# Kernel optimization log

Measured on AMD Instinct MI355X. Metric: run time of the kernel, lower is better.

The kernel has to match this reference:

```python
import jax, jax.numpy as jnp
import numpy as np

B, E, DIN, H, D, T = 16, 512, 1024, 8, 128, 3
NEG = -1e30
LRELU_SLOPE = 0.2


def setup_inputs() -> dict:
    key = jax.random.key(0)
    ks = jax.random.split(key, 6)
    x = jax.random.normal(ks[0], (B, E, DIN), dtype=jnp.float32)
    adj = jax.random.randint(ks[1], (B, E, E), 0, 4, dtype=jnp.int32)  # 0=no edge, 1..3 edge types
    node_mask = jnp.ones((B, E, 1), dtype=jnp.float32)
    W = jax.random.normal(ks[2], (H, T, DIN, D), dtype=jnp.float32) * 0.02
    a1 = jax.random.normal(ks[3], (H, T, D), dtype=jnp.float32) * 0.02  # a[:d]
    a2 = jax.random.normal(ks[4], (H, T, D), dtype=jnp.float32) * 0.02  # a[d:]
    return {"x": x, "adj": adj, "node_mask": node_mask, "W": W, "a1": a1, "a2": a2}


def reference(x, adj, node_mask, W, a1, a2):
    # h per head/type: [H, T, B, E, D]
    h = jnp.einsum('bei,htid->htbed', x, W)
    # a(cat(h_i, h_j)) = h_i . a1 + h_j . a2 (linear, no bias)
    left = jnp.einsum('htbed,htd->htbe', h, a1)   # [H,T,B,E]
    right = jnp.einsum('htbed,htd->htbe', h, a2)  # [H,T,B,E]
    score = left[..., :, None] + right[..., None, :]             # [H,T,B,E,E]
    score = jnp.where(score > 0, score, LRELU_SLOPE * score)      # LeakyReLU(0.2)
    type_ids = (jnp.arange(T, dtype=adj.dtype) + 1).reshape(1, T, 1, 1, 1)
    # sum over types: only positions where adj == type contribute
    scores = jnp.sum(jnp.where(adj[None, None] == type_ids, score, 0.0), axis=1)  # [H,B,E,E]
    scores = jnp.where(adj[None] > 0, scores, NEG)
    coefs = jax.nn.softmax(scores, axis=-1)                       # [H,B,E,E]
    # original bug (faithful): h used in aggregation is from the LAST edge type
    h_last = h[:, -1] * node_mask[None]                           # [H,B,E,D]
    out = jnp.einsum('hbef,hbfd->hbed', coefs, h_last)            # [H,B,E,D]
    out = jnp.transpose(out, (1, 2, 0, 3)).reshape(B, E, H * D)   # concat heads
    return jax.nn.relu(out)
```

## Files before the change

### kernel.cpp

```cpp
#include <hip/hip_runtime.h>

typedef __attribute__((ext_vector_type(8))) _Float16 half8;
typedef __attribute__((ext_vector_type(8))) unsigned short u16x8;
typedef __attribute__((ext_vector_type(4))) unsigned short u16x4;
typedef __attribute__((ext_vector_type(4))) float f32x4;

#define NEGV (-1e30f)


__device__ __forceinline__ unsigned short f2h(float f) {
    union { _Float16 h; unsigned short u; } c;
    c.h = (_Float16)f;
    return c.u;
}
__device__ __forceinline__ float h2f(unsigned short u) {
    union { _Float16 h; unsigned short u; } c;
    c.u = u;
    return (float)c.h;
}

__global__ __launch_bounds__(256) void prep_kernel(const int* __restrict__ adj,
                                                   const float* __restrict__ W,
                                                   const float* __restrict__ a1,
                                                   const float* __restrict__ a2,
                                                   unsigned short* __restrict__ Bf,
                                                   unsigned char* __restrict__ adjB) {
    __shared__ float tile[64 * 133];
    const int bid = blockIdx.x;
    const int tid = threadIdx.x;

    if (bid < 1024) {
        const int idx = bid * 256 + tid;
        const int4* s = (const int4*)(adj + (size_t)idx * 16);
        int4 v0 = s[0], v1 = s[1], v2 = s[2], v3 = s[3];
        union { unsigned char c[16]; int4 v; } o;
        o.c[0] = (unsigned char)v0.x; o.c[1] = (unsigned char)v0.y;
        o.c[2] = (unsigned char)v0.z; o.c[3] = (unsigned char)v0.w;
        o.c[4] = (unsigned char)v1.x; o.c[5] = (unsigned char)v1.y;
        o.c[6] = (unsigned char)v1.z; o.c[7] = (unsigned char)v1.w;
        o.c[8] = (unsigned char)v2.x; o.c[9] = (unsigned char)v2.y;
        o.c[10] = (unsigned char)v2.z; o.c[11] = (unsigned char)v2.w;
        o.c[12] = (unsigned char)v3.x; o.c[13] = (unsigned char)v3.y;
        o.c[14] = (unsigned char)v3.z; o.c[15] = (unsigned char)v3.w;
        *(int4*)(adjB + (size_t)idx * 16) = o.v;
    } else if (bid < 1152) {
        const int pb = bid - 1024;
        const int kt = pb & 15, h = pb >> 4;
        const int k0 = kt * 64;
        const float* wsrc = W + ((size_t)((h * 3 + 2) * 1024) + k0) * 128;

        #pragma unroll
        for (int rep = 0; rep < 8; ++rep) {
            int idx = rep * 256 + tid;
            int k = idx >> 5, dc = (idx & 31) * 4;
            float4 v = *(const float4*)(wsrc + (size_t)k * 128 + dc);
            tile[k * 133 + dc + 0] = v.x;
            tile[k * 133 + dc + 1] = v.y;
            tile[k * 133 + dc + 2] = v.z;
            tile[k * 133 + dc + 3] = v.w;
        }
        __syncthreads();
        #pragma unroll
        for (int rep = 0; rep < 4; ++rep) {
            int idx = rep * 256 + tid;
            int d = idx >> 3, kc = (idx & 7) * 8;
            u16x8 vh;
            #pragma unroll
            for (int q = 0; q < 8; ++q) vh[q] = f2h(tile[(kc + q) * 133 + d]);
            *(u16x8*)(Bf + (size_t)(h * 128 + d) * 1024 + k0 + kc) = vh;
        }
    } else if (bid < 1536) {
        const int pb = bid - 1152;
        const int kt = pb & 15, ht = pb >> 4;
        const int h = ht & 7, t = ht >> 3;
        const int k0 = kt * 64;
        const float* wsrc = W + ((size_t)((h * 3 + t) * 1024) + k0) * 128;

        #pragma unroll
        for (int rep = 0; rep < 8; ++rep) {
            int idx = rep * 256 + tid;
            int k = idx >> 5, dc = (idx & 31) * 4;
            float4 v = *(const float4*)(wsrc + (size_t)k * 128 + dc);
            tile[k * 133 + dc + 0] = v.x;
            tile[k * 133 + dc + 1] = v.y;
            tile[k * 133 + dc + 2] = v.z;
            tile[k * 133 + dc + 3] = v.w;
        }
        __syncthreads();
        if (tid < 128) {
            const int k = tid & 63, s = tid >> 6;
            const float* ar = (s ? a2 : a1) + (h * 3 + t) * 128;
            float acc = 0.f;
            #pragma unroll 4
            for (int d = 0; d < 128; ++d) acc += tile[k * 133 + d] * ar[d];
            Bf[(size_t)(1024 + s * 24 + t * 8 + h) * 1024 + k0 + k] = f2h(acc);
        }
    } else {
        const int n = 1072 + (bid - 1536);
        *(unsigned long long*)(Bf + (size_t)n * 1024 + tid * 4) = 0ull;
    }
}

__global__ __launch_bounds__(256, 3) void mgemm(const float* __restrict__ X,
                                                const unsigned short* __restrict__ Bf,
                                                const float* __restrict__ nm,
                                                unsigned short* __restrict__ Vt,
                                                float* __restrict__ LR) {
    __shared__ unsigned short Ah[2][128 * 32];
    __shared__ unsigned short Bfs[2][128 * 32];

    const int bid = blockIdx.x;
    const int swz = (bid & 7) * 72 + (bid >> 3);
    const int nt = swz % 9, mt = swz / 9;
    const int n0 = nt * 128, m0 = mt * 128;

    const int tid = threadIdx.x;
    const int lane = tid & 63, w = tid >> 6;
    const int wr = w >> 1, wc = w & 1;
    const int fr = lane & 15, fq = lane >> 4;

    f32x4 acc[4][4];
    #pragma unroll
    for (int m = 0; m < 4; ++m)
        #pragma unroll
        for (int n = 0; n < 4; ++n) acc[m][n] = (f32x4){0.f, 0.f, 0.f, 0.f};

    const int arow = tid >> 1, ahalf = tid & 1;
    const float* xs = X + (size_t)(m0 + arow) * 1024 + ahalf * 16;
    const int aoff = arow * 32 + ahalf * 16;

#define GLDB(kk, buf) do {                                                        \
        _Pragma("unroll")                                                          \
        for (int q_ = 0; q_ < 2; ++q_) {                                           \
            const int s_ = q_ * 256 + tid;                                         \
            const int brow_ = s_ >> 2, bkb_ = s_ & 3;                              \
            const unsigned short* g_ = Bf + (size_t)(n0 + brow_) * 1024 + (kk) + bkb_ * 8; \
            unsigned short* d_ = &Bfs[buf][(q_ * 256 + w * 64) * 8];               \
            __builtin_amdgcn_global_load_lds(                                      \
                (const __attribute__((address_space(1))) void*)g_,                 \
                (__attribute__((address_space(3))) void*)d_, 16, 0, 0);            \
        }                                                                          \
    } while (0)

#define CONVA(xa_, xb_, xc_, xd_, buf) do {                                       \
        float xf_[16] = {(xa_).x, (xa_).y, (xa_).z, (xa_).w,                       \
                         (xb_).x, (xb_).y, (xb_).z, (xb_).w,                       \
                         (xc_).x, (xc_).y, (xc_).z, (xc_).w,                       \
                         (xd_).x, (xd_).y, (xd_).z, (xd_).w};                      \
        u16x8 v0_, v1_;                                                            \
        _Pragma("unroll")                                                          \
        for (int i_ = 0; i_ < 8; ++i_) v0_[i_] = f2h(xf_[i_]);                     \
        _Pragma("unroll")                                                          \
        for (int i_ = 0; i_ < 8; ++i_) v1_[i_] = f2h(xf_[8 + i_]);                 \
        *(u16x8*)(&Ah[buf][aoff]) = v0_;                                           \
        *(u16x8*)(&Ah[buf][aoff + 8]) = v1_;                                       \
    } while (0)

    GLDB(0, 0);
    {
        float4 xa = *(const float4*)(xs);
        float4 xb = *(const float4*)(xs + 4);
        float4 xc = *(const float4*)(xs + 8);
        float4 xd = *(const float4*)(xs + 12);
        CONVA(xa, xb, xc, xd, 0);
    }
    __syncthreads();

    for (int k0 = 0; k0 < 1024; k0 += 32) {
        const int cur = (k0 >> 5) & 1;
        const int nxt = cur ^ 1;
        const bool more = (k0 < 992);

        float4 xa, xb, xc, xd;
        if (more) {
            GLDB(k0 + 32, nxt);
            xa = *(const float4*)(xs + k0 + 32);
            xb = *(const float4*)(xs + k0 + 36);
            xc = *(const float4*)(xs + k0 + 40);
            xd = *(const float4*)(xs + k0 + 44);
        }

        half8 am[4], bn[4];
        #pragma unroll
        for (int m = 0; m < 4; ++m)
            am[m] = *(half8*)(&Ah[cur][(wr * 64 + m * 16 + fr) * 32 + fq * 8]);
        #pragma unroll
        for (int n = 0; n < 4; ++n)
            bn[n] = *(half8*)(&Bfs[cur][(wc * 64 + n * 16 + fr) * 32 + fq * 8]);
        #pragma unroll
        for (int m = 0; m < 4; ++m)
            #pragma unroll
            for (int n = 0; n < 4; ++n)
                acc[m][n] = __builtin_amdgcn_mfma_f32_16x16x32_f16(am[m], bn[n], acc[m][n], 0, 0, 0);

        if (more) {
            CONVA(xa, xb, xc, xd, nxt);
        }

        __syncthreads();
    }
#undef GLDB
#undef CONVA

    if (nt < 8) {
        const int b_ = (mt * 128) >> 9;
        const int jb0 = (mt & 3) * 128;
        unsigned short* vtw = Vt + (size_t)(nt * 16 + b_) * 128 * 512;
        #pragma unroll
        for (int m = 0; m < 4; ++m) {
            const int jb = jb0 + wr * 64 + m * 16 + fq * 4;
            float mk[4];
            #pragma unroll
            for (int r = 0; r < 4; ++r)
                mk[r] = nm[m0 + wr * 64 + m * 16 + fq * 4 + r];
            #pragma unroll
            for (int n = 0; n < 4; ++n) {
                const int d = wc * 64 + n * 16 + fr;
                u16x4 pk;
                #pragma unroll
                for (int r = 0; r < 4; ++r) pk[r] = f2h(acc[m][n][r] * mk[r]);
                *(u16x4*)(vtw + (size_t)d * 512 + jb) = pk;
            }
        }
    } else {
        #pragma unroll
        for (int m = 0; m < 4; ++m) {
            #pragma unroll
            for (int r = 0; r < 4; ++r) {
                const int R = m0 + wr * 64 + m * 16 + fq * 4 + r;
                #pragma unroll
                for (int n = 0; n < 4; ++n) {
                    const int c = wc * 64 + n * 16 + fr;
                    if (c < 48) LR[(size_t)c * 8192 + R] = acc[m][n][r];
                }
            }
        }
    }
}

__global__ __launch_bounds__(256, 4) void attn_kernel(const unsigned short* __restrict__ Vt,
                                                      const float* __restrict__ LR,
                                                      const unsigned char* __restrict__ adjB,
                                                      float* __restrict__ out) {
    __shared__ __align__(16) unsigned short Vb[2][16 * 512];
    __shared__ __align__(16) float rt[3 * 512];

    const int bid = blockIdx.x;
    const int itg = bid >> 7, hb = bid & 127, h = hb >> 4, b = hb & 15;
    const int tid = threadIdx.x, w = tid >> 6, lane = tid & 63;
    const int fr = lane & 15, fq = lane >> 4;
    const int i0 = (itg * 4 + w) * 16;
    const int fq8 = fq * 8;

    for (int idx = tid; idx < 1536; idx += 256) {
        int t = idx >> 9, j = idx & 511;
        rt[idx] = LR[(size_t)(24 + t * 8 + h) * 8192 + b * 512 + j];
    }
    const float lf0 = LR[(size_t)(h) * 8192 + b * 512 + i0 + fr];
    const float lf1 = LR[(size_t)(8 + h) * 8192 + b * 512 + i0 + fr];
    const float lf2 = LR[(size_t)(16 + h) * 8192 + b * 512 + i0 + fr];
    const unsigned char* arow = adjB + (size_t)(b * 512 + i0 + fr) * 512;
    const unsigned short* vt = Vt + (size_t)(h * 16 + b) * 128 * 512;

#define STAGE_V(bufp, os_) do {                                                   \
        _Pragma("unroll")                                                          \
        for (int q_ = 0; q_ < 4; ++q_) {                                           \
            const int nh_ = q_ * 4 + w;                                            \
            const unsigned short* src_ = vt + (size_t)((nh_ >> 1) * 16 + fr) * 512 \
                                          + (os_) * 64 + (nh_ & 1) * 32 + fq8;     \
            unsigned short* dst_ = (bufp) + nh_ * 512;                             \
            __builtin_amdgcn_global_load_lds(                                      \
                (const __attribute__((address_space(1))) void*)src_,               \
                (__attribute__((address_space(3))) void*)dst_, 16, 0, 0);          \
        }                                                                          \
    } while (0)

    STAGE_V(&Vb[0][0], 0);
    uint2 aA = *(const uint2*)(arow + fq8);
    uint2 aB = *(const uint2*)(arow + fq8 + 32);

    f32x4 acc[8];
    #pragma unroll
    for (int n = 0; n < 8; ++n) acc[n] = (f32x4){0.f, 0.f, 0.f, 0.f};
    float rsum = 0.f;

    __syncthreads();

    #pragma unroll 1
    for (int os = 0; os < 8; ++os) {
        unsigned short* vb = &Vb[os & 1][0];
        if (os < 7) STAGE_V(&Vb[(os & 1) ^ 1][0], os + 1);

        const int jA = os * 64 + fq8;
        const int jB = jA + 32;

        u16x8 vhA, vhB;
        {
            float4 r0a = *(const float4*)(rt + jA), r0b = *(const float4*)(rt + jA + 4);
            float4 r1a = *(const float4*)(rt + 512 + jA), r1b = *(const float4*)(rt + 512 + jA + 4);
            float4 r2a = *(const float4*)(rt + 1024 + jA), r2b = *(const float4*)(rt + 1024 + jA + 4);
            float e0[8] = {r0a.x, r0a.y, r0a.z, r0a.w, r0b.x, r0b.y, r0b.z, r0b.w};
            float e1[8] = {r1a.x, r1a.y, r1a.z, r1a.w, r1b.x, r1b.y, r1b.z, r1b.w};
            float e2[8] = {r2a.x, r2a.y, r2a.z, r2a.w, r2b.x, r2b.y, r2b.z, r2b.w};
            #pragma unroll
            for (int q = 0; q < 8; ++q) {
                unsigned av = ((q < 4 ? aA.x : aA.y) >> (8 * (q & 3))) & 255u;
                float sb = (av == 1u) ? (lf0 + e0[q])
                         : (av == 2u) ? (lf1 + e1[q]) : (lf2 + e2[q]);
                float sv = fmaxf(sb, 0.f) + 0.2f * fminf(sb, 0.f);
                float p = (av != 0u) ? __expf(sv) : 0.f;
                rsum += p;
                vhA[q] = f2h(p);
            }
        }
        {
            float4 r0a = *(const float4*)(rt + jB), r0b = *(const float4*)(rt + jB + 4);
            float4 r1a = *(const float4*)(rt + 512 + jB), r1b = *(const float4*)(rt + 512 + jB + 4);
            float4 r2a = *(const float4*)(rt + 1024 + jB), r2b = *(const float4*)(rt + 1024 + jB + 4);
            float e0[8] = {r0a.x, r0a.y, r0a.z, r0a.w, r0b.x, r0b.y, r0b.z, r0b.w};
            float e1[8] = {r1a.x, r1a.y, r1a.z, r1a.w, r1b.x, r1b.y, r1b.z, r1b.w};
            float e2[8] = {r2a.x, r2a.y, r2a.z, r2a.w, r2b.x, r2b.y, r2b.z, r2b.w};
            #pragma unroll
            for (int q = 0; q < 8; ++q) {
                unsigned av = ((q < 4 ? aB.x : aB.y) >> (8 * (q & 3))) & 255u;
                float sb = (av == 1u) ? (lf0 + e0[q])
                         : (av == 2u) ? (lf1 + e1[q]) : (lf2 + e2[q]);
                float sv = fmaxf(sb, 0.f) + 0.2f * fminf(sb, 0.f);
                float p = (av != 0u) ? __expf(sv) : 0.f;
                rsum += p;
                vhB[q] = f2h(p);
            }
        }
        if (os < 7) {
            aA = *(const uint2*)(arow + (os + 1) * 64 + fq8);
            aB = *(const uint2*)(arow + (os + 1) * 64 + fq8 + 32);
        }

        half8 ahA = *(half8*)&vhA, ahB = *(half8*)&vhB;

        #pragma unroll
        for (int n = 0; n < 8; ++n) {
            half8 vA = *(half8*)(vb + (n * 2 + 0) * 512 + lane * 8);
            half8 vB = *(half8*)(vb + (n * 2 + 1) * 512 + lane * 8);
            acc[n] = __builtin_amdgcn_mfma_f32_16x16x32_f16(ahA, vA, acc[n], 0, 0, 0);
            acc[n] = __builtin_amdgcn_mfma_f32_16x16x32_f16(ahB, vB, acc[n], 0, 0, 0);
        }
        __syncthreads();
    }
#undef STAGE_V

    rsum += __shfl_xor(rsum, 16);
    rsum += __shfl_xor(rsum, 32);

    #pragma unroll
    for (int rr = 0; rr < 4; ++rr) {
        const int row = fq * 4 + rr;
        const float inv = 1.0f / __shfl(rsum, row);
        #pragma unroll
        for (int n = 0; n < 8; ++n) {
            out[(size_t)(b * 512 + i0 + row) * 1024 + h * 128 + n * 16 + fr] =
                fmaxf(acc[n][rr] * inv, 0.f);
        }
    }
}

extern "C" void kernel_launch(void* const* d_in, const int* in_sizes, int n_in,
                              void* d_out, int out_size, void* d_ws, size_t ws_size,
                              hipStream_t stream) {
    const float* x   = (const float*)d_in[0];
    const int*   adj = (const int*)d_in[1];
    const float* nm  = (const float*)d_in[2];
    const float* W   = (const float*)d_in[3];
    const float* a1  = (const float*)d_in[4];
    const float* a2  = (const float*)d_in[5];
    float* out = (float*)d_out;
    char* wsb = (char*)d_ws;

    unsigned short* Bf   = (unsigned short*)(wsb);
    float*          LR   = (float*)(wsb + 21495808);
    unsigned short* Vt   = (unsigned short*)(wsb + 23068672);
    unsigned char*  adjB = (unsigned char*)(wsb + 39845888);

    hipLaunchKernelGGL(prep_kernel, dim3(1616), dim3(256), 0, stream, adj, W, a1, a2, Bf, adjB);
    hipLaunchKernelGGL(mgemm, dim3(576), dim3(256), 0, stream, x, Bf, nm, Vt, LR);
    hipLaunchKernelGGL(attn_kernel, dim3(1024), dim3(256), 0, stream, Vt, LR, adjB, out);
}
```

Before: 108.6 us.

## Unroll GEMM K-loop by two with register-prefetched x and partial vmcnt barriers

Restructures the projection GEMM main loop into a manually unrolled two-stage pipeline with static buffer indices. The x fp32 loads are now issued one stage further ahead, into a second register set. __syncthreads is replaced by inline s_waitcnt vmcnt(4) plus s_barrier, so the x loads still in flight need not drain at every barrier. sched_barrier fences pin instruction order. This aims to hide global-load latency behind the MFMAs, at the cost of more VGPRs and a fragile hand-counted vmcnt that must match the number of outstanding loads.

```diff
diff --git a/kernel.cpp b/kernel.cpp
--- a/kernel.cpp
+++ b/kernel.cpp
@@ -156,51 +156,76 @@
         *(u16x8*)(&Ah[buf][aoff + 8]) = v1_;                                       \
     } while (0)
 
+#define COMPUTE(buf) do {                                                         \
+        half8 am_[4], bn_[4];                                                      \
+        _Pragma("unroll")                                                          \
+        for (int m_ = 0; m_ < 4; ++m_)                                             \
+            am_[m_] = *(half8*)(&Ah[buf][(wr * 64 + m_ * 16 + fr) * 32 + fq * 8]); \
+        _Pragma("unroll")                                                          \
+        for (int n_ = 0; n_ < 4; ++n_)                                             \
+            bn_[n_] = *(half8*)(&Bfs[buf][(wc * 64 + n_ * 16 + fr) * 32 + fq * 8]);\
+        _Pragma("unroll")                                                          \
+        for (int m_ = 0; m_ < 4; ++m_)                                             \
+            _Pragma("unroll")                                                      \
+            for (int n_ = 0; n_ < 4; ++n_)                                         \
+                acc[m_][n_] = __builtin_amdgcn_mfma_f32_16x16x32_f16(am_[m_], bn_[n_], acc[m_][n_], 0, 0, 0); \
+    } while (0)
+
+#define PIPE_BAR4() asm volatile("s_waitcnt vmcnt(4) lgkmcnt(0)\n\ts_barrier" ::: "memory")
+#define PIPE_BAR0() asm volatile("s_waitcnt vmcnt(0) lgkmcnt(0)\n\ts_barrier" ::: "memory")
+
+    float4 x0a, x0b, x0c, x0d, x1a, x1b, x1c, x1d;
+
+    x0a = *(const float4*)(xs);
+    x0b = *(const float4*)(xs + 4);
+    x0c = *(const float4*)(xs + 8);
+    x0d = *(const float4*)(xs + 12);
+    __builtin_amdgcn_sched_barrier(0);
     GLDB(0, 0);
-    {
-        float4 xa = *(const float4*)(xs);
-        float4 xb = *(const float4*)(xs + 4);
-        float4 xc = *(const float4*)(xs + 8);
-        float4 xd = *(const float4*)(xs + 12);
-        CONVA(xa, xb, xc, xd, 0);
-    }
-    __syncthreads();
-
-    for (int k0 = 0; k0 < 1024; k0 += 32) {
-        const int cur = (k0 >> 5) & 1;
-        const int nxt = cur ^ 1;
-        const bool more = (k0 < 992);
-
-        float4 xa, xb, xc, xd;
-        if (more) {
-            GLDB(k0 + 32, nxt);
-            xa = *(const float4*)(xs + k0 + 32);
-            xb = *(const float4*)(xs + k0 + 36);
-            xc = *(const float4*)(xs + k0 + 40);
-            xd = *(const float4*)(xs + k0 + 44);
-        }
-
-        half8 am[4], bn[4];
-        #pragma unroll
-        for (int m = 0; m < 4; ++m)
-            am[m] = *(half8*)(&Ah[cur][(wr * 64 + m * 16 + fr) * 32 + fq * 8]);
-        #pragma unroll
-        for (int n = 0; n < 4; ++n)
-            bn[n] = *(half8*)(&Bfs[cur][(wc * 64 + n * 16 + fr) * 32 + fq * 8]);
-        #pragma unroll
-        for (int m = 0; m < 4; ++m)
-            #pragma unroll
-            for (int n = 0; n < 4; ++n)
-                acc[m][n] = __builtin_amdgcn_mfma_f32_16x16x32_f16(am[m], bn[n], acc[m][n], 0, 0, 0);
-
-        if (more) {
-            CONVA(xa, xb, xc, xd, nxt);
-        }
-
-        __syncthreads();
-    }
+    __builtin_amdgcn_sched_barrier(0);
+    CONVA(x0a, x0b, x0c, x0d, 0);
+    x1a = *(const float4*)(xs + 32);
+    x1b = *(const float4*)(xs + 36);
+    x1c = *(const float4*)(xs + 40);
+    x1d = *(const float4*)(xs + 44);
+    PIPE_BAR4();
+
+    for (int kk = 0; kk < 928; kk += 64) {
+        GLDB(kk + 32, 1);
+        __builtin_amdgcn_sched_barrier(0);
+        x0a = *(const float4*)(xs + kk + 64);
+        x0b = *(const float4*)(xs + kk + 68);
+        x0c = *(const float4*)(xs + kk + 72);
+        x0d = *(const float4*)(xs + kk + 76);
+        __builtin_amdgcn_sched_barrier(0);
+        COMPUTE(0);
+        CONVA(x1a, x1b, x1c, x1d, 1);
+        PIPE_BAR4();
+
+        GLDB(kk + 64, 0);
+        __builtin_amdgcn_sched_barrier(0);
+        x1a = *(const float4*)(xs + kk + 96);
+        x1b = *(const float4*)(xs + kk + 100);
+        x1c = *(const float4*)(xs + kk + 104);
+        x1d = *(const float4*)(xs + kk + 108);
+        __builtin_amdgcn_sched_barrier(0);
+        COMPUTE(1);
+        CONVA(x0a, x0b, x0c, x0d, 0);
+        PIPE_BAR4();
+    }
+
+    GLDB(992, 1);
+    __builtin_amdgcn_sched_barrier(0);
+    COMPUTE(0);
+    CONVA(x1a, x1b, x1c, x1d, 1);
+    PIPE_BAR0();
+    COMPUTE(1);
+
 #undef GLDB
 #undef CONVA
+#undef COMPUTE
+#undef PIPE_BAR4
+#undef PIPE_BAR0
 
     if (nt < 8) {
         const int b_ = (mt * 128) >> 9;
```

After: 97.40 us (median of 3 runs). -10.3%, faster.
